# Optimization experiments

Measured on AMD Instinct MI355X. Metric: run time of the kernel, lower is better.

## Reference

```python
import jax, jax.numpy as jnp
import numpy as np

HIDDEN = 2048
NUM_HEADS = 16
NUM_KV_HEADS = 4
HEAD_DIM = HIDDEN // NUM_HEADS  # 128
ROPE_THETA = 1000000.0
B, S = 2, 2048


def setup_inputs() -> dict:
    key = jax.random.key(0)
    ks = jax.random.split(key, 10)
    sc = 0.02
    return {
        "hidden_states": jax.random.normal(ks[0], (B, S, HIDDEN), jnp.float32),
        "position_ids": jnp.broadcast_to(jnp.arange(S, dtype=jnp.int32), (B, S)),
        "Wq": jax.random.normal(ks[1], (HIDDEN, NUM_HEADS * HEAD_DIM), jnp.float32) * sc,
        "bq": jnp.zeros((NUM_HEADS * HEAD_DIM,), jnp.float32),
        "Wk": jax.random.normal(ks[2], (HIDDEN, NUM_KV_HEADS * HEAD_DIM), jnp.float32) * sc,
        "bk": jnp.zeros((NUM_KV_HEADS * HEAD_DIM,), jnp.float32),
        "Wv": jax.random.normal(ks[3], (HIDDEN, NUM_KV_HEADS * HEAD_DIM), jnp.float32) * sc,
        "bv": jnp.zeros((NUM_KV_HEADS * HEAD_DIM,), jnp.float32),
        "Wo": jax.random.normal(ks[4], (NUM_HEADS * HEAD_DIM, HIDDEN), jnp.float32) * sc,
        "bo": jnp.zeros((HIDDEN,), jnp.float32),
    }


def _rope_cos_sin(position_ids, dtype):
    # inv_freq: [head_dim/2]
    inv_freq = 1.0 / (ROPE_THETA ** (jnp.arange(0, HEAD_DIM, 2, dtype=jnp.float32) / HEAD_DIM))
    freqs = position_ids.astype(jnp.float32)[:, :, None] * inv_freq[None, None, :]  # [B,S,d/2]
    emb = jnp.concatenate([freqs, freqs], axis=-1)  # [B,S,d]
    return jnp.cos(emb).astype(dtype), jnp.sin(emb).astype(dtype)


def _rotate_half(x):
    h = x.shape[-1] // 2
    return jnp.concatenate([-x[..., h:], x[..., :h]], axis=-1)


def _attention(hidden_states, position_ids, Wq, bq, Wk, bk, Wv, bv, Wo, bo):
    bsz, q_len, _ = hidden_states.shape
    q = (hidden_states @ Wq + bq).reshape(bsz, q_len, NUM_HEADS, HEAD_DIM).transpose(0, 2, 1, 3)
    k = (hidden_states @ Wk + bk).reshape(bsz, q_len, NUM_KV_HEADS, HEAD_DIM).transpose(0, 2, 1, 3)
    v = (hidden_states @ Wv + bv).reshape(bsz, q_len, NUM_KV_HEADS, HEAD_DIM).transpose(0, 2, 1, 3)

    cos, sin = _rope_cos_sin(position_ids, hidden_states.dtype)
    cos = cos[:, None, :, :]  # [B,1,S,d]
    sin = sin[:, None, :, :]
    q = q * cos + _rotate_half(q) * sin
    k = k * cos + _rotate_half(k) * sin

    # repeat_kv (GQA): [B,kvh,S,d] -> [B,H,S,d]
    n_rep = NUM_HEADS // NUM_KV_HEADS
    k = jnp.repeat(k, n_rep, axis=1)
    v = jnp.repeat(v, n_rep, axis=1)

    scale = 1.0 / jnp.sqrt(jnp.array(HEAD_DIM, hidden_states.dtype))
    scores = jnp.einsum('bhqd,bhkd->bhqk', q, k) * scale  # [B,H,S,S]
    causal = jnp.tril(jnp.ones((q_len, q_len), bool))
    scores = jnp.where(causal[None, None], scores, jnp.finfo(scores.dtype).min)
    probs = jax.nn.softmax(scores.astype(jnp.float32), axis=-1).astype(hidden_states.dtype)
    attn = jnp.einsum('bhqk,bhkd->bhqd', probs, v)
    attn = attn.transpose(0, 2, 1, 3).reshape(bsz, q_len, HIDDEN)
    return attn @ Wo + bo


def reference(hidden_states, position_ids, Wq, bq, Wk, bk, Wv, bv, Wo, bo):
    return _attention(hidden_states, position_ids, Wq, bq, Wk, bk, Wv, bv, Wo, bo)
```

## Files before the change

### kernel.cpp

```cpp
#include <hip/hip_runtime.h>
#include <cmath>

#define HIDDEN 2048
#define NH 16
#define NKV 4
#define HD 128
#define SEQ 2048
#define BATCH 2

typedef unsigned short ushort_t;
typedef short bf16x8 __attribute__((ext_vector_type(8)));
typedef float f32x4 __attribute__((ext_vector_type(4)));
typedef ushort_t u16x4 __attribute__((ext_vector_type(4)));

__device__ __forceinline__ ushort_t f2bf(float f) {
    union { float f; unsigned int u; } v; v.f = f;
    unsigned int r = v.u + 0x7fffu + ((v.u >> 16) & 1u);
    return (ushort_t)(r >> 16);
}
__device__ __forceinline__ ushort_t f2bf_trunc(float f) {
    union { float f; unsigned int u; } v; v.f = f;
    return (ushort_t)(v.u >> 16);
}

__device__ __forceinline__ f32x4 mfma16(bf16x8 a, bf16x8 b, f32x4 c) {
    return __builtin_amdgcn_mfma_f32_16x16x32_bf16(a, b, c, 0, 0, 0);
}

__device__ __forceinline__ void load_lds16(const void* g, void* l) {
    __builtin_amdgcn_global_load_lds((const __attribute__((address_space(1))) unsigned int*)g,
                                     (__attribute__((address_space(3))) unsigned int*)l,
                                     16, 0, 0);
}

__global__ __launch_bounds__(256) void convert_x(const float* __restrict__ x,
                                                 ushort_t* __restrict__ xb, int n4) {
    int g = blockIdx.x * 256 + threadIdx.x;
    if (g >= n4) return;
    float4 v = ((const float4*)x)[g];
    u16x4 o;
    o[0] = f2bf(v.x); o[1] = f2bf(v.y); o[2] = f2bf(v.z); o[3] = f2bf(v.w);
    ((u16x4*)xb)[g] = o;
}

__global__ __launch_bounds__(256) void transpose_all(const float* __restrict__ Wq,
                                                     const float* __restrict__ Wk,
                                                     const float* __restrict__ Wv,
                                                     const float* __restrict__ Wo,
                                                     ushort_t* __restrict__ WqkvT,
                                                     ushort_t* __restrict__ WoT) {
    const int z = blockIdx.z;
    const float* W;
    ushort_t* WT;
    int N;
    if (z == 0)      { W = Wq; WT = WqkvT;                        N = 2048; }
    else if (z == 1) { W = Wk; WT = WqkvT + 2048ull * 2048;       N = 512;  }
    else if (z == 2) { W = Wv; WT = WqkvT + 2560ull * 2048;       N = 512;  }
    else             { W = Wo; WT = WoT;                          N = 2048; }
    const int K = 2048;
    const int n0 = blockIdx.x * 64, k0 = blockIdx.y * 64;
    if (n0 >= N) return;
    __shared__ ushort_t T[64][72];
    const int t = threadIdx.x;
    for (int idx = t; idx < 64 * 16; idx += 256) {
        int r = idx >> 4, c4 = (idx & 15) << 2;
        float4 v = *(const float4*)&W[(size_t)(k0 + r) * N + n0 + c4];
        T[r][c4 + 0] = f2bf(v.x); T[r][c4 + 1] = f2bf(v.y);
        T[r][c4 + 2] = f2bf(v.z); T[r][c4 + 3] = f2bf(v.w);
    }
    __syncthreads();
    for (int idx = t; idx < 64 * 16; idx += 256) {
        int n = idx >> 4, kg = (idx & 15) << 2;
        u16x4 o;
        o[0] = T[kg + 0][n]; o[1] = T[kg + 1][n];
        o[2] = T[kg + 2][n]; o[3] = T[kg + 3][n];
        *(u16x4*)&WT[(size_t)(n0 + n) * K + k0 + kg] = o;
    }
}

template <int MODE>
__global__ __launch_bounds__(512) void gemm256(const ushort_t* __restrict__ A,
                                               const ushort_t* __restrict__ Bt,
                                               const float* __restrict__ bias,
                                               const float* __restrict__ bias2,
                                               const float* __restrict__ bias3,
                                               void* __restrict__ out,
                                               void* __restrict__ out2,
                                               void* __restrict__ out3,
                                               int M, int N, int K,
                                               const int* __restrict__ posids) {
    __shared__ __align__(16) ushort_t Asb[2][16384];
    __shared__ __align__(16) ushort_t Bsb[2][16384];
    const int tid = threadIdx.x;
    const int w = tid >> 6, lane = tid & 63, quad = lane >> 4, l16 = lane & 15;
    const int wr = w >> 2, wc = w & 3;
    const int m0 = blockIdx.y * 256, n0 = blockIdx.x * 256;

    f32x4 acc[8][4];
#pragma unroll
    for (int i = 0; i < 8; i++)
#pragma unroll
        for (int j = 0; j < 4; j++)
#pragma unroll
            for (int e = 0; e < 4; e++) acc[i][j][e] = 0.0f;

    const int lrow = lane >> 3;
    const int kh_s = ((lane >> 2) & 1) ^ ((lane >> 3) & 1);
    const int c_s  = (lane & 3) ^ ((lane >> 4) & 3);
    const int scol = kh_s * 32 + c_s * 8;

    auto stageA = [&](int t, int buf, int ha) {
        const ushort_t* g = A + (size_t)(m0 + ha * 128 + w * 16 + lrow) * K + t * 64 + scol;
        ushort_t* l = &Asb[buf][(ha * 128 + w * 16) * 64];
        load_lds16(g, l);
        load_lds16(g + (size_t)8 * K, l + 512);
    };
    auto stageB = [&](int t, int buf, int ha) {
        const ushort_t* g = Bt + (size_t)(n0 + ha * 128 + w * 16 + lrow) * K + t * 64 + scol;
        ushort_t* l = &Bsb[buf][(ha * 128 + w * 16) * 64];
        load_lds16(g, l);
        load_lds16(g + (size_t)8 * K, l + 512);
    };

    const int sw = (quad ^ ((l16 >> 1) & 3)) * 8;
    const int off0 = ((l16 & 1) ? 32 : 0) + sw;
    const int off1 = ((l16 & 1) ? 0 : 32) + sw;
    const int arow = (wr * 128 + l16) * 64;
    const int brow = (wc * 16 + l16) * 64;

    const int nt = K >> 6;

    stageA(0, 0, 0); stageA(0, 0, 1); stageB(0, 0, 0); stageB(0, 0, 1);
    asm volatile("s_waitcnt vmcnt(2)" ::: "memory");
    __builtin_amdgcn_s_barrier();
    __builtin_amdgcn_sched_barrier(0);

    bf16x8 a[8];
    for (int u = 0; u < nt; ++u) {
        const int bu = u & 1, bn = bu ^ 1;
        const bool pf = (u + 1 < nt);
        const ushort_t* Ab = Asb[bu];
        const ushort_t* Bb = Bsb[bu];

#pragma unroll
        for (int i = 0; i < 8; i++) a[i] = *(const bf16x8*)&Ab[arow + i * 1024 + off0];
        bf16x8 b0 = *(const bf16x8*)&Bb[brow + off0];
        bf16x8 b1 = *(const bf16x8*)&Bb[brow + 4096 + off0];
        if (pf) { stageA(u + 1, bn, 0); asm volatile("s_waitcnt vmcnt(2)" ::: "memory"); }
        else    { asm volatile("s_waitcnt vmcnt(0)" ::: "memory"); }
        __builtin_amdgcn_s_barrier();
        __builtin_amdgcn_sched_barrier(0);
        __builtin_amdgcn_s_setprio(1);
#pragma unroll
        for (int i = 0; i < 8; i++) {
            acc[i][0] = mfma16(a[i], b0, acc[i][0]);
            acc[i][1] = mfma16(a[i], b1, acc[i][1]);
        }
        __builtin_amdgcn_s_setprio(0);
        __builtin_amdgcn_sched_barrier(0);
        __builtin_amdgcn_s_barrier();
        __builtin_amdgcn_sched_barrier(0);

        bf16x8 b2 = *(const bf16x8*)&Bb[brow + 8192 + off0];
        bf16x8 b3 = *(const bf16x8*)&Bb[brow + 12288 + off0];
        if (pf) stageA(u + 1, bn, 1);
        __builtin_amdgcn_s_barrier();
        __builtin_amdgcn_sched_barrier(0);
        __builtin_amdgcn_s_setprio(1);
#pragma unroll
        for (int i = 0; i < 8; i++) {
            acc[i][2] = mfma16(a[i], b2, acc[i][2]);
            acc[i][3] = mfma16(a[i], b3, acc[i][3]);
        }
        __builtin_amdgcn_s_setprio(0);
        __builtin_amdgcn_sched_barrier(0);
        __builtin_amdgcn_s_barrier();
        __builtin_amdgcn_sched_barrier(0);

#pragma unroll
        for (int i = 0; i < 8; i++) a[i] = *(const bf16x8*)&Ab[arow + i * 1024 + off1];
        b0 = *(const bf16x8*)&Bb[brow + off1];
        b1 = *(const bf16x8*)&Bb[brow + 4096 + off1];
        if (pf) stageB(u + 1, bn, 0);
        __builtin_amdgcn_s_barrier();
        __builtin_amdgcn_sched_barrier(0);
        __builtin_amdgcn_s_setprio(1);
#pragma unroll
        for (int i = 0; i < 8; i++) {
            acc[i][0] = mfma16(a[i], b0, acc[i][0]);
            acc[i][1] = mfma16(a[i], b1, acc[i][1]);
        }
        __builtin_amdgcn_s_setprio(0);
        __builtin_amdgcn_sched_barrier(0);
        __builtin_amdgcn_s_barrier();
        __builtin_amdgcn_sched_barrier(0);

        b2 = *(const bf16x8*)&Bb[brow + 8192 + off1];
        b3 = *(const bf16x8*)&Bb[brow + 12288 + off1];
        if (pf) { stageB(u + 1, bn, 1); asm volatile("s_waitcnt vmcnt(2)" ::: "memory"); }
        __builtin_amdgcn_s_barrier();
        __builtin_amdgcn_sched_barrier(0);
        __builtin_amdgcn_s_setprio(1);
#pragma unroll
        for (int i = 0; i < 8; i++) {
            acc[i][2] = mfma16(a[i], b2, acc[i][2]);
            acc[i][3] = mfma16(a[i], b3, acc[i][3]);
        }
        __builtin_amdgcn_s_setprio(0);
        __builtin_amdgcn_sched_barrier(0);
        __builtin_amdgcn_s_barrier();
        __builtin_amdgcn_sched_barrier(0);
    }

    if (MODE == 0) {
        float* O = (float*)out;
#pragma unroll
        for (int i = 0; i < 8; i++)
#pragma unroll
            for (int r = 0; r < 4; r++) {
                int row = m0 + wr * 128 + i * 16 + quad * 4 + r;
#pragma unroll
                for (int j = 0; j < 4; j++) {
                    int col = n0 + (wc + 4 * j) * 16 + l16;
                    O[(size_t)row * N + col] = acc[i][j][r] + bias[col];
                }
            }
    } else {
        if (n0 < 2048) {
            ushort_t* O = (ushort_t*)out;
            const int h0 = n0 >> 7;
            const float scale = 0.08838834764831845f;
            const int dl = wc * 16 + l16;
            const float fr = __expf(-0.21586735246819178f * (float)dl);
#pragma unroll
            for (int i = 0; i < 8; i++)
#pragma unroll
                for (int r = 0; r < 4; r++) {
                    int row = m0 + wr * 128 + i * 16 + quad * 4 + r;
                    int b = row >> 11, s = row & (SEQ - 1);
                    float pos = (float)posids[row];
                    float sn, cs;
                    __sincosf(pos * fr, &sn, &cs);
#pragma unroll
                    for (int p = 0; p < 2; p++) {
                        float x1 = acc[i][2 * p][r] + bias[n0 + p * 128 + dl];
                        float x2 = acc[i][2 * p + 1][r] + bias[n0 + p * 128 + dl + 64];
                        size_t obase = ((size_t)(b * NH + h0 + p) * SEQ + s) * HD;
                        O[obase + dl]      = f2bf((x1 * cs - x2 * sn) * scale);
                        O[obase + dl + 64] = f2bf((x2 * cs + x1 * sn) * scale);
                    }
                }
        } else if (n0 < 2560) {
            ushort_t* O = (ushort_t*)out2;
            const int n0k = n0 - 2048;
            const int h0 = n0k >> 7;
            const int dl = wc * 16 + l16;
            const float fr = __expf(-0.21586735246819178f * (float)dl);
#pragma unroll
            for (int i = 0; i < 8; i++)
#pragma unroll
                for (int r = 0; r < 4; r++) {
                    int row = m0 + wr * 128 + i * 16 + quad * 4 + r;
                    int b = row >> 11, s = row & (SEQ - 1);
                    float pos = (float)posids[row];
                    float sn, cs;
                    __sincosf(pos * fr, &sn, &cs);
#pragma unroll
                    for (int p = 0; p < 2; p++) {
                        float x1 = acc[i][2 * p][r] + bias2[n0k + p * 128 + dl];
                        float x2 = acc[i][2 * p + 1][r] + bias2[n0k + p * 128 + dl + 64];
                        size_t obase = ((size_t)(b * NKV + h0 + p) * SEQ + s) * HD;
                        O[obase + dl]      = f2bf(x1 * cs - x2 * sn);
                        O[obase + dl + 64] = f2bf(x2 * cs + x1 * sn);
                    }
                }
        } else {
            ushort_t* O = (ushort_t*)out3;
            const int n0v = n0 - 2560;
#pragma unroll
            for (int i = 0; i < 8; i++)
#pragma unroll
                for (int r = 0; r < 4; r++) {
                    int row = m0 + wr * 128 + i * 16 + quad * 4 + r;
                    int b = row >> 11, s = row & (SEQ - 1);
#pragma unroll
                    for (int j = 0; j < 4; j++) {
                        int ct = wc + 4 * j;
                        int h = (n0v >> 7) + (ct >> 3);
                        int d = (ct & 7) * 16 + l16;
                        float v = acc[i][j][r] + bias3[n0v + ct * 16 + l16];
                        O[((size_t)(b * NKV + h) * HD + d) * SEQ + s] = f2bf(v);
                    }
                }
        }
    }
}

__global__ __launch_bounds__(256) void flash(const ushort_t* __restrict__ Qr,
                                             const ushort_t* __restrict__ Kr,
                                             const ushort_t* __restrict__ Vt,
                                             ushort_t* __restrict__ Attn) {
    __shared__ __align__(16) ushort_t Ksh[2 * 4 * 64 * 32];
    __shared__ __align__(16) ushort_t Vsh[2 * 2 * 128 * 32];
    __shared__ __align__(16) ushort_t Ps[4 * 16 * 72];
    const int tid = threadIdx.x;
    const int w = tid >> 6, lane = tid & 63, quad = lane >> 4, l16 = lane & 15;
    const int x = blockIdx.x, h = blockIdx.y, b = blockIdx.z;
    const int qt = b ? x : (gridDim.x - 1 - x);
    const int q0 = qt * 128;
    const int nkt = 2 * qt + 2;
    const int hkv = h >> 2;
    const ushort_t* Kg = Kr + ((size_t)(b * NKV + hkv) * SEQ) * HD;
    const ushort_t* Vg = Vt + ((size_t)(b * NKV + hkv) * HD) * SEQ;

    const int p = lane >> 2;
    const int gc8 = (((lane & 3) ^ ((lane >> 3) & 3)) << 3);
    const ushort_t* kst = Kg + (size_t)p * HD + w * 32 + gc8;
    const ushort_t* vst = Vg + (size_t)((w & 1) * 64 + p) * SEQ + (w >> 1) * 32 + gc8;
    ushort_t* ksl = Ksh + w * 2048;
    ushort_t* vsl = Vsh + (w >> 1) * 4096 + (w & 1) * 2048;

    auto stage = [&](int bi, int kv0) {
        const ushort_t* gk = kst + (size_t)kv0 * HD;
        ushort_t* lk = ksl + bi * 8192;
        load_lds16(gk, lk);
        load_lds16(gk + (size_t)16 * HD, lk + 512);
        load_lds16(gk + (size_t)32 * HD, lk + 1024);
        load_lds16(gk + (size_t)48 * HD, lk + 1536);
        const ushort_t* gv = vst + kv0;
        ushort_t* lv = vsl + bi * 8192;
        load_lds16(gv, lv);
        load_lds16(gv + (size_t)16 * SEQ, lv + 512);
        load_lds16(gv + (size_t)32 * SEQ, lv + 1024);
        load_lds16(gv + (size_t)48 * SEQ, lv + 1536);
    };

    bf16x8 aq[2][4];
#pragma unroll
    for (int st = 0; st < 2; st++) {
        const size_t qrow = ((size_t)(b * NH + h) * SEQ + q0 + st * 64 + w * 16 + l16) * HD;
#pragma unroll
        for (int kc = 0; kc < 4; kc++)
            aq[st][kc] = *(const bf16x8*)&Qr[qrow + kc * 32 + quad * 8];
    }

    f32x4 o[2][8];
#pragma unroll
    for (int st = 0; st < 2; st++)
#pragma unroll
        for (int j = 0; j < 8; j++)
#pragma unroll
            for (int e = 0; e < 4; e++) o[st][j][e] = 0.0f;
    f32x4 ls2[2];
#pragma unroll
    for (int st = 0; st < 2; st++)
        for (int e = 0; e < 4; e++) ls2[st][e] = 0.0f;
    bf16x8 ones;
#pragma unroll
    for (int e = 0; e < 8; e++) ones[e] = (short)0x3F80;

    ushort_t* Pw = &Ps[w * 16 * 72];
    const int rsw8 = ((l16 >> 1) & 3) << 3;

    stage(0, 0);
    asm volatile("s_waitcnt vmcnt(0)" ::: "memory");
    __builtin_amdgcn_s_barrier();

    for (int kt = 0; kt < nkt; kt++) {
        const int kv0 = kt * 64;
        const int cur = kt & 1;
        if (kt + 1 < nkt) {
            stage(cur ^ 1, kv0 + 64);
            asm volatile("s_waitcnt vmcnt(8)" ::: "memory");
        } else {
            asm volatile("s_waitcnt vmcnt(0)" ::: "memory");
        }
        __builtin_amdgcn_s_barrier();

        const ushort_t* Kb = Ksh + cur * 8192;
        const ushort_t* Vb = Vsh + cur * 8192;

#pragma unroll
        for (int st = 0; st < 2; st++) {
            if (st == 0 && kt == 2 * qt + 1) continue;

            f32x4 sa[4];
#pragma unroll
            for (int nt = 0; nt < 4; nt++)
#pragma unroll
                for (int e = 0; e < 4; e++) sa[nt][e] = 0.0f;
#pragma unroll
            for (int kc = 0; kc < 4; kc++) {
#pragma unroll
                for (int nt = 0; nt < 4; nt++) {
                    bf16x8 bk = *(const bf16x8*)&Kb[kc * 2048 + nt * 512 + l16 * 32 +
                                                    ((quad * 8) ^ rsw8)];
                    sa[nt] = mfma16(aq[st][kc], bk, sa[nt]);
                }
            }

            if ((kt >> 1) == qt && (kt & 1) == st) {
#pragma unroll
                for (int nt = 0; nt < 4; nt++)
#pragma unroll
                    for (int r = 0; r < 4; r++) {
                        int kvg = kv0 + nt * 16 + l16;
                        int qg = q0 + st * 64 + w * 16 + quad * 4 + r;
                        if (kvg > qg) sa[nt][r] = -1e30f;
                    }
            }

#pragma unroll
            for (int nt = 0; nt < 4; nt++)
#pragma unroll
                for (int r = 0; r < 4; r++)
                    Pw[(quad * 4 + r) * 72 + nt * 16 + l16] = f2bf_trunc(__expf(sa[nt][r]));

#pragma unroll
            for (int kc = 0; kc < 2; kc++) {
                bf16x8 ap = *(const bf16x8*)&Pw[l16 * 72 + kc * 32 + quad * 8];
                ls2[st] = mfma16(ap, ones, ls2[st]);
#pragma unroll
                for (int j = 0; j < 8; j++) {
                    bf16x8 bv = *(const bf16x8*)&Vb[kc * 4096 + (j * 16 + l16) * 32 +
                                                    ((quad * 8) ^ rsw8)];
                    o[st][j] = mfma16(ap, bv, o[st][j]);
                }
            }
        }
        asm volatile("s_barrier" ::: "memory");
    }

#pragma unroll
    for (int st = 0; st < 2; st++)
#pragma unroll
        for (int r = 0; r < 4; r++) {
            float inv = 1.0f / ls2[st][r];
            int row = b * SEQ + q0 + st * 64 + w * 16 + quad * 4 + r;
            size_t obase = (size_t)row * HIDDEN + h * HD;
#pragma unroll
            for (int j = 0; j < 8; j++) Attn[obase + j * 16 + l16] = f2bf(o[st][j][r] * inv);
        }
}

extern "C" void kernel_launch(void* const* d_in, const int* in_sizes, int n_in,
                              void* d_out, int out_size, void* d_ws, size_t ws_size,
                              hipStream_t stream) {
    const float* hs = (const float*)d_in[0];
    const int* posids = (const int*)d_in[1];
    const float* Wq = (const float*)d_in[2];
    const float* bq = (const float*)d_in[3];
    const float* Wk = (const float*)d_in[4];
    const float* bk = (const float*)d_in[5];
    const float* Wv = (const float*)d_in[6];
    const float* bv = (const float*)d_in[7];
    const float* Wo = (const float*)d_in[8];
    const float* bo = (const float*)d_in[9];
    float* out = (float*)d_out;

    char* ws = (char*)d_ws;
    size_t off = 0;
    auto alloc = [&](size_t bytes) {
        char* p = ws + off;
        off += (bytes + 255) & ~(size_t)255;
        return p;
    };
    ushort_t* Xb     = (ushort_t*)alloc(4096ull * 2048 * 2);
    ushort_t* WqkvT  = (ushort_t*)alloc(3072ull * 2048 * 2);
    ushort_t* WoT    = (ushort_t*)alloc(2048ull * 2048 * 2);
    ushort_t* Qr     = (ushort_t*)alloc((size_t)BATCH * NH * SEQ * HD * 2);
    ushort_t* Kr     = (ushort_t*)alloc((size_t)BATCH * NKV * SEQ * HD * 2);
    ushort_t* Vtr    = (ushort_t*)alloc((size_t)BATCH * NKV * HD * SEQ * 2);
    ushort_t* Attn   = (ushort_t*)alloc(4096ull * 2048 * 2);

    convert_x<<<4096 * 2048 / 4 / 256, 256, 0, stream>>>(hs, Xb, 4096 * 2048 / 4);
    transpose_all<<<dim3(32, 32, 4), 256, 0, stream>>>(Wq, Wk, Wv, Wo, WqkvT, WoT);

    gemm256<2><<<dim3(12, 16), 512, 0, stream>>>(Xb, WqkvT, bq, bk, bv,
                                                 Qr, Kr, Vtr, 4096, 3072, 2048, posids);

    flash<<<dim3(SEQ / 128, NH, BATCH), 256, 0, stream>>>(Qr, Kr, Vtr, Attn);

    gemm256<0><<<dim3(8, 16), 512, 0, stream>>>(Attn, WoT, bo, nullptr, nullptr,
                                                out, nullptr, nullptr, 4096, 2048, 2048, nullptr);
}
```

Measured before the change: 343.7 us.

## Balance causal flash work by pairing q-tiles and halve output GEMM M-tile

```diff
diff --git a/kernel.cpp b/kernel.cpp
--- a/kernel.cpp
+++ b/kernel.cpp
@@ -78,7 +78,7 @@
     }
 }
 
-template <int MODE>
+template <int MODE, int BMH>
 __global__ __launch_bounds__(512) void gemm256(const ushort_t* __restrict__ A,
                                                const ushort_t* __restrict__ Bt,
                                                const float* __restrict__ bias,
@@ -89,16 +89,17 @@
                                                void* __restrict__ out3,
                                                int M, int N, int K,
                                                const int* __restrict__ posids) {
-    __shared__ __align__(16) ushort_t Asb[2][16384];
+    constexpr int IM = 4 * BMH;
+    __shared__ __align__(16) ushort_t Asb[2][BMH * 8192];
     __shared__ __align__(16) ushort_t Bsb[2][16384];
     const int tid = threadIdx.x;
     const int w = tid >> 6, lane = tid & 63, quad = lane >> 4, l16 = lane & 15;
     const int wr = w >> 2, wc = w & 3;
-    const int m0 = blockIdx.y * 256, n0 = blockIdx.x * 256;
-
-    f32x4 acc[8][4];
-#pragma unroll
-    for (int i = 0; i < 8; i++)
+    const int m0 = blockIdx.y * (128 * BMH), n0 = blockIdx.x * 256;
+
+    f32x4 acc[IM][4];
+#pragma unroll
+    for (int i = 0; i < IM; i++)
 #pragma unroll
         for (int j = 0; j < 4; j++)
 #pragma unroll
@@ -125,17 +126,20 @@
     const int sw = (quad ^ ((l16 >> 1) & 3)) * 8;
     const int off0 = ((l16 & 1) ? 32 : 0) + sw;
     const int off1 = ((l16 & 1) ? 0 : 32) + sw;
-    const int arow = (wr * 128 + l16) * 64;
+    const int arow = (wr * (64 * BMH) + l16) * 64;
     const int brow = (wc * 16 + l16) * 64;
 
     const int nt = K >> 6;
 
-    stageA(0, 0, 0); stageA(0, 0, 1); stageB(0, 0, 0); stageB(0, 0, 1);
+    stageA(0, 0, 0);
+    if constexpr (BMH == 2) stageA(0, 0, 1);
+    stageB(0, 0, 0);
+    stageB(0, 0, 1);
     asm volatile("s_waitcnt vmcnt(2)" ::: "memory");
     __builtin_amdgcn_s_barrier();
     __builtin_amdgcn_sched_barrier(0);
 
-    bf16x8 a[8];
+    bf16x8 a[IM];
     for (int u = 0; u < nt; ++u) {
         const int bu = u & 1, bn = bu ^ 1;
         const bool pf = (u + 1 < nt);
@@ -143,7 +147,7 @@
         const ushort_t* Bb = Bsb[bu];
 
 #pragma unroll
-        for (int i = 0; i < 8; i++) a[i] = *(const bf16x8*)&Ab[arow + i * 1024 + off0];
+        for (int i = 0; i < IM; i++) a[i] = *(const bf16x8*)&Ab[arow + i * 1024 + off0];
         bf16x8 b0 = *(const bf16x8*)&Bb[brow + off0];
         bf16x8 b1 = *(const bf16x8*)&Bb[brow + 4096 + off0];
         if (pf) { stageA(u + 1, bn, 0); asm volatile("s_waitcnt vmcnt(2)" ::: "memory"); }
@@ -152,7 +156,7 @@
         __builtin_amdgcn_sched_barrier(0);
         __builtin_amdgcn_s_setprio(1);
 #pragma unroll
-        for (int i = 0; i < 8; i++) {
+        for (int i = 0; i < IM; i++) {
             acc[i][0] = mfma16(a[i], b0, acc[i][0]);
             acc[i][1] = mfma16(a[i], b1, acc[i][1]);
         }
@@ -163,12 +167,15 @@
 
         bf16x8 b2 = *(const bf16x8*)&Bb[brow + 8192 + off0];
         bf16x8 b3 = *(const bf16x8*)&Bb[brow + 12288 + off0];
-        if (pf) stageA(u + 1, bn, 1);
+        if (pf) {
+            if constexpr (BMH == 2) stageA(u + 1, bn, 1);
+            else                    stageB(u + 1, bn, 0);
+        }
         __builtin_amdgcn_s_barrier();
         __builtin_amdgcn_sched_barrier(0);
         __builtin_amdgcn_s_setprio(1);
 #pragma unroll
-        for (int i = 0; i < 8; i++) {
+        for (int i = 0; i < IM; i++) {
             acc[i][2] = mfma16(a[i], b2, acc[i][2]);
             acc[i][3] = mfma16(a[i], b3, acc[i][3]);
         }
@@ -178,15 +185,18 @@
         __builtin_amdgcn_sched_barrier(0);
 
 #pragma unroll
-        for (int i = 0; i < 8; i++) a[i] = *(const bf16x8*)&Ab[arow + i * 1024 + off1];
+        for (int i = 0; i < IM; i++) a[i] = *(const bf16x8*)&Ab[arow + i * 1024 + off1];
         b0 = *(const bf16x8*)&Bb[brow + off1];
         b1 = *(const bf16x8*)&Bb[brow + 4096 + off1];
-        if (pf) stageB(u + 1, bn, 0);
+        if (pf) {
+            if constexpr (BMH == 2) stageB(u + 1, bn, 0);
+            else                    stageB(u + 1, bn, 1);
+        }
         __builtin_amdgcn_s_barrier();
         __builtin_amdgcn_sched_barrier(0);
         __builtin_amdgcn_s_setprio(1);
 #pragma unroll
-        for (int i = 0; i < 8; i++) {
+        for (int i = 0; i < IM; i++) {
             acc[i][0] = mfma16(a[i], b0, acc[i][0]);
             acc[i][1] = mfma16(a[i], b1, acc[i][1]);
         }
@@ -197,12 +207,15 @@
 
         b2 = *(const bf16x8*)&Bb[brow + 8192 + off1];
         b3 = *(const bf16x8*)&Bb[brow + 12288 + off1];
-        if (pf) { stageB(u + 1, bn, 1); asm volatile("s_waitcnt vmcnt(2)" ::: "memory"); }
+        if (pf) {
+            if constexpr (BMH == 2) stageB(u + 1, bn, 1);
+            asm volatile("s_waitcnt vmcnt(2)" ::: "memory");
+        }
         __builtin_amdgcn_s_barrier();
         __builtin_amdgcn_sched_barrier(0);
         __builtin_amdgcn_s_setprio(1);
 #pragma unroll
-        for (int i = 0; i < 8; i++) {
+        for (int i = 0; i < IM; i++) {
             acc[i][2] = mfma16(a[i], b2, acc[i][2]);
             acc[i][3] = mfma16(a[i], b3, acc[i][3]);
         }
@@ -215,10 +228,10 @@
     if (MODE == 0) {
         float* O = (float*)out;
 #pragma unroll
-        for (int i = 0; i < 8; i++)
+        for (int i = 0; i < IM; i++)
 #pragma unroll
             for (int r = 0; r < 4; r++) {
-                int row = m0 + wr * 128 + i * 16 + quad * 4 + r;
+                int row = m0 + wr * (64 * BMH) + i * 16 + quad * 4 + r;
 #pragma unroll
                 for (int j = 0; j < 4; j++) {
                     int col = n0 + (wc + 4 * j) * 16 + l16;
@@ -233,10 +246,10 @@
             const int dl = wc * 16 + l16;
             const float fr = __expf(-0.21586735246819178f * (float)dl);
 #pragma unroll
-            for (int i = 0; i < 8; i++)
+            for (int i = 0; i < IM; i++)
 #pragma unroll
                 for (int r = 0; r < 4; r++) {
-                    int row = m0 + wr * 128 + i * 16 + quad * 4 + r;
+                    int row = m0 + wr * (64 * BMH) + i * 16 + quad * 4 + r;
                     int b = row >> 11, s = row & (SEQ - 1);
                     float pos = (float)posids[row];
                     float sn, cs;
@@ -257,10 +270,10 @@
             const int dl = wc * 16 + l16;
             const float fr = __expf(-0.21586735246819178f * (float)dl);
 #pragma unroll
-            for (int i = 0; i < 8; i++)
+            for (int i = 0; i < IM; i++)
 #pragma unroll
                 for (int r = 0; r < 4; r++) {
-                    int row = m0 + wr * 128 + i * 16 + quad * 4 + r;
+                    int row = m0 + wr * (64 * BMH) + i * 16 + quad * 4 + r;
                     int b = row >> 11, s = row & (SEQ - 1);
                     float pos = (float)posids[row];
                     float sn, cs;
@@ -278,10 +291,10 @@
             ushort_t* O = (ushort_t*)out3;
             const int n0v = n0 - 2560;
 #pragma unroll
-            for (int i = 0; i < 8; i++)
+            for (int i = 0; i < IM; i++)
 #pragma unroll
                 for (int r = 0; r < 4; r++) {
-                    int row = m0 + wr * 128 + i * 16 + quad * 4 + r;
+                    int row = m0 + wr * (64 * BMH) + i * 16 + quad * 4 + r;
                     int b = row >> 11, s = row & (SEQ - 1);
 #pragma unroll
                     for (int j = 0; j < 4; j++) {
@@ -306,9 +319,8 @@
     const int tid = threadIdx.x;
     const int w = tid >> 6, lane = tid & 63, quad = lane >> 4, l16 = lane & 15;
     const int x = blockIdx.x, h = blockIdx.y, b = blockIdx.z;
-    const int qt = b ? x : (gridDim.x - 1 - x);
-    const int q0 = qt * 128;
-    const int nkt = 2 * qt + 2;
+    const int qa = x, qb = 31 - x;
+    const int nkt = qb + 1;
     const int hkv = h >> 2;
     const ushort_t* Kg = Kr + ((size_t)(b * NKV + hkv) * SEQ) * HD;
     const ushort_t* Vg = Vt + ((size_t)(b * NKV + hkv) * HD) * SEQ;
@@ -338,7 +350,8 @@
     bf16x8 aq[2][4];
 #pragma unroll
     for (int st = 0; st < 2; st++) {
-        const size_t qrow = ((size_t)(b * NH + h) * SEQ + q0 + st * 64 + w * 16 + l16) * HD;
+        const int qst = st ? qb : qa;
+        const size_t qrow = ((size_t)(b * NH + h) * SEQ + qst * 64 + w * 16 + l16) * HD;
 #pragma unroll
         for (int kc = 0; kc < 4; kc++)
             aq[st][kc] = *(const bf16x8*)&Qr[qrow + kc * 32 + quad * 8];
@@ -382,7 +395,8 @@
 
 #pragma unroll
         for (int st = 0; st < 2; st++) {
-            if (st == 0 && kt == 2 * qt + 1) continue;
+            const int qst = st ? qb : qa;
+            if (st == 0 && kt > qa) continue;
 
             f32x4 sa[4];
 #pragma unroll
@@ -399,13 +413,13 @@
                 }
             }
 
-            if ((kt >> 1) == qt && (kt & 1) == st) {
+            if (kt == qst) {
 #pragma unroll
                 for (int nt = 0; nt < 4; nt++)
 #pragma unroll
                     for (int r = 0; r < 4; r++) {
                         int kvg = kv0 + nt * 16 + l16;
-                        int qg = q0 + st * 64 + w * 16 + quad * 4 + r;
+                        int qg = qst * 64 + w * 16 + quad * 4 + r;
                         if (kvg > qg) sa[nt][r] = -1e30f;
                     }
             }
@@ -432,15 +446,17 @@
     }
 
 #pragma unroll
-    for (int st = 0; st < 2; st++)
+    for (int st = 0; st < 2; st++) {
+        const int qst = st ? qb : qa;
 #pragma unroll
         for (int r = 0; r < 4; r++) {
             float inv = 1.0f / ls2[st][r];
-            int row = b * SEQ + q0 + st * 64 + w * 16 + quad * 4 + r;
+            int row = b * SEQ + qst * 64 + w * 16 + quad * 4 + r;
             size_t obase = (size_t)row * HIDDEN + h * HD;
 #pragma unroll
             for (int j = 0; j < 8; j++) Attn[obase + j * 16 + l16] = f2bf(o[st][j][r] * inv);
         }
+    }
 }
 
 extern "C" void kernel_launch(void* const* d_in, const int* in_sizes, int n_in,
@@ -476,11 +492,11 @@
     convert_x<<<4096 * 2048 / 4 / 256, 256, 0, stream>>>(hs, Xb, 4096 * 2048 / 4);
     transpose_all<<<dim3(32, 32, 4), 256, 0, stream>>>(Wq, Wk, Wv, Wo, WqkvT, WoT);
 
-    gemm256<2><<<dim3(12, 16), 512, 0, stream>>>(Xb, WqkvT, bq, bk, bv,
-                                                 Qr, Kr, Vtr, 4096, 3072, 2048, posids);
-
-    flash<<<dim3(SEQ / 128, NH, BATCH), 256, 0, stream>>>(Qr, Kr, Vtr, Attn);
-
-    gemm256<0><<<dim3(8, 16), 512, 0, stream>>>(Attn, WoT, bo, nullptr, nullptr,
-                                                out, nullptr, nullptr, 4096, 2048, 2048, nullptr);
-}
+    gemm256<2, 2><<<dim3(12, 16), 512, 0, stream>>>(Xb, WqkvT, bq, bk, bv,
+                                                    Qr, Kr, Vtr, 4096, 3072, 2048, posids);
+
+    flash<<<dim3(16, NH, BATCH), 256, 0, stream>>>(Qr, Kr, Vtr, Attn);
+
+    gemm256<0, 1><<<dim3(8, 32), 512, 0, stream>>>(Attn, WoT, bo, nullptr, nullptr,
+                                                   out, nullptr, nullptr, 4096, 2048, 2048, nullptr);
+}
```

Result: faster. 314.9 us (-8.4%).
